# Performance work log

Measured on AMD Instinct MI355X. Metric: run time of the kernel, lower is better.

## Reference

```python
import jax, jax.numpy as jnp
import numpy as np

B, T, D = 16, 2048, 128   # batch, seq_len, input_size
H, L = 256, 2             # hidden_size, rnn layers
N1, N2 = 32, 32           # head output sizes


def _rnn_dir(x, Wih, Whh, bih, bhh, reverse):
    # x: [B, T, din] -> outputs [B, T, H]; torch RNN tanh cell:
    # h_t = tanh(W_ih x_t + b_ih + W_hh h_{t-1} + b_hh), h_0 = 0
    xT = jnp.swapaxes(x, 0, 1)            # [T, B, din]
    if reverse:
        xT = xT[::-1]
    pre = xT @ Wih.T + (bih + bhh)        # batch input projection once
    h0 = jnp.zeros((x.shape[0], Whh.shape[0]), x.dtype)
    def step(h, u):
        h = jnp.tanh(u + h @ Whh.T)
        return h, h
    _, hs = jax.lax.scan(step, h0, pre)   # [T, B, H]
    if reverse:
        hs = hs[::-1]
    return jnp.swapaxes(hs, 0, 1)         # [B, T, H]


def _birnn(x, params):
    out = x
    for l in range(L):
        Wf, Uf, bf, cf, Wb, Ub, bb, cb = params[l]
        fwd = _rnn_dir(out, Wf, Uf, bf, cf, reverse=False)
        bwd = _rnn_dir(out, Wb, Ub, bb, cb, reverse=True)
        out = jnp.concatenate([fwd, bwd], axis=-1)  # [B, T, 2H]
    return out


def _head(h, W1, b1, W2, b2):
    # fc1 -> relu -> fc2, fully batched over [B, T]
    z = jax.nn.relu(jnp.einsum('bth,kh->btk', h, W1) + b1)
    return jnp.einsum('btk,nk->btn', z, W2) + b2


def setup_inputs() -> dict:
    key = jax.random.key(0)
    ks = iter(jax.random.split(key, 40))
    def p(shape):
        return jax.random.normal(next(ks), shape, jnp.float32) * 0.05
    inp = {"x": jax.random.normal(next(ks), (B, T, D), jnp.float32)}
    for l in range(L):
        din = D if l == 0 else 2 * H
        for d in ("f", "b"):
            inp[f"Wih{l}{d}"] = p((H, din))
            inp[f"Whh{l}{d}"] = p((H, H))
            inp[f"bih{l}{d}"] = p((H,))
            inp[f"bhh{l}{d}"] = p((H,))
    for t, n in (("t1", N1), ("t2", N2)):
        inp[f"W1{t}"] = p((H // 2, 2 * H))
        inp[f"b1{t}"] = p((H // 2,))
        inp[f"W2{t}"] = p((n, H // 2))
        inp[f"b2{t}"] = p((n,))
    return inp


def reference(x,
              Wih0f, Whh0f, bih0f, bhh0f, Wih0b, Whh0b, bih0b, bhh0b,
              Wih1f, Whh1f, bih1f, bhh1f, Wih1b, Whh1b, bih1b, bhh1b,
              W1t1, b1t1, W2t1, b2t1, W1t2, b1t2, W2t2, b2t2):
    params = [
        (Wih0f, Whh0f, bih0f, bhh0f, Wih0b, Whh0b, bih0b, bhh0b),
        (Wih1f, Whh1f, bih1f, bhh1f, Wih1b, Whh1b, bih1b, bhh1b),
    ]
    out = _birnn(x, params)                       # [B, T, 2H]
    y1 = _head(out, W1t1, b1t1, W2t1, b2t1)       # [B, T, N1]
    y2 = _head(out, W1t2, b1t2, W2t2, b2t2)       # [B, T, N2]
    return (y1, y2)
```

## Files before the change

kernel.cpp:

```cpp
#include <hip/hip_runtime.h>
#include <hip/hip_fp16.h>

typedef _Float16 half2_t __attribute__((ext_vector_type(2)));
typedef _Float16 half8_t __attribute__((ext_vector_type(8)));
typedef float f32x4 __attribute__((ext_vector_type(4)));

struct __align__(16) H2x4 { half2_t h[4]; };

__device__ __forceinline__ float fdot2f(half2_t a, half2_t b, float c){
#if __has_builtin(__builtin_amdgcn_fdot2)
  return __builtin_amdgcn_fdot2(a, b, c, false);
#else
  return c + (float)a[0]*(float)b[0] + (float)a[1]*(float)b[1];
#endif
}

__device__ __forceinline__ float fast_exp2f(float x){
#if __has_builtin(__builtin_amdgcn_exp2f)
  return __builtin_amdgcn_exp2f(x);
#else
  return __expf(x*0.6931471805599453f);
#endif
}

struct PrepArgs {
  const float* src[13];
  __half* dst[13];
  int n[13];
};
__global__ __launch_bounds__(256) void prep_cast_k(PrepArgs a){
  const int r = blockIdx.y;
  const int n = a.n[r];
  const float* __restrict__ s = a.src[r];
  __half* __restrict__ d = a.dst[r];
  for (int i = blockIdx.x*256 + threadIdx.x; i < n; i += gridDim.x*256)
    d[i] = __float2half(s[i]);
}

struct BiasArgs {
  const float *bih0f,*bhh0f,*bih0b,*bhh0b,*bih1f,*bhh1f,*bih1b,*bhh1b;
  const float *b1t1,*b1t2,*b2t1,*b2t2;
  float *b0,*b1,*bz,*by;
};
__global__ __launch_bounds__(256) void prep_bias_k(BiasArgs a){
  const int i = threadIdx.x;
  if (i < 256){
    a.b0[i]     = a.bih0f[i] + a.bhh0f[i];
    a.b0[256+i] = a.bih0b[i] + a.bhh0b[i];
    a.b1[i]     = a.bih1f[i] + a.bhh1f[i];
    a.b1[256+i] = a.bih1b[i] + a.bhh1b[i];
  }
  if (i < 128){ a.bz[i] = a.b1t1[i]; a.bz[128+i] = a.b1t2[i]; }
  if (i < 32){  a.by[i] = a.b2t1[i]; a.by[32+i]  = a.b2t2[i]; }
}

template<bool RELU>
__global__ __launch_bounds__(256,2) void gemm_nt_k(
    const __half* __restrict__ A, const __half* __restrict__ B,
    __half* __restrict__ C, const float* __restrict__ bias,
    int M, int N, int K, long dirStride)
{
  __shared__ __align__(16) _Float16 As[128*40];
  __shared__ __align__(16) _Float16 Bs[128*40];
  const int tid = threadIdx.x;
  const int wave = tid>>6, lane = tid&63;
  const int wr = wave>>1, wc = wave&1;
  const int lrow = lane&15, lk = lane>>4;
  const int m0 = blockIdx.x*128, n0 = blockIdx.y*128;
  f32x4 acc[4][4];
  #pragma unroll
  for (int i=0;i<4;i++)
    #pragma unroll
    for (int j=0;j<4;j++) acc[i][j] = (f32x4){0.f,0.f,0.f,0.f};

  for (int k0=0; k0<K; k0+=32){
    __syncthreads();
    #pragma unroll
    for (int i=0;i<2;i++){
      int idx = i*256 + tid;
      int row = idx>>2, ch = idx&3;
      const int4 av = *(const int4*)(A + (size_t)(m0+row)*K + k0 + ch*8);
      const int4 bv = *(const int4*)(B + (size_t)(n0+row)*K + k0 + ch*8);
      *(int4*)(As + row*40 + ch*8) = av;
      *(int4*)(Bs + row*40 + ch*8) = bv;
    }
    __syncthreads();
    half8_t af[4], bf[4];
    #pragma unroll
    for (int mi=0;mi<4;mi++) af[mi] = *(const half8_t*)(As + (wr*64+mi*16+lrow)*40 + lk*8);
    #pragma unroll
    for (int ni=0;ni<4;ni++) bf[ni] = *(const half8_t*)(Bs + (wc*64+ni*16+lrow)*40 + lk*8);
    #pragma unroll
    for (int mi=0;mi<4;mi++)
      #pragma unroll
      for (int ni=0;ni<4;ni++)
        acc[mi][ni] = __builtin_amdgcn_mfma_f32_16x16x32_f16(af[mi], bf[ni], acc[mi][ni], 0,0,0);
  }
  #pragma unroll
  for (int mi=0;mi<4;mi++){
    #pragma unroll
    for (int ni=0;ni<4;ni++){
      const int n = n0 + wc*64 + ni*16 + lrow;
      const float bv = bias[n];
      const size_t base = (size_t)(n>>8)*dirStride + (size_t)(n&255);
      #pragma unroll
      for (int r2=0;r2<4;r2++){
        const int m = m0 + wr*64 + mi*16 + lk*4 + r2;
        float v = acc[mi][ni][r2] + bv;
        if (RELU) v = fmaxf(v, 0.f);
        C[(size_t)m*256 + base] = __float2half(v);
      }
    }
  }
}

__global__ __launch_bounds__(256,1) void rnn_layer_k(
    const __half* __restrict__ pre, const __half* __restrict__ whh,
    __half* __restrict__ out, int T)
{
  const int dir = blockIdx.x >> 4;
  const int batch = blockIdx.x & 15;
  const int tid = threadIdx.x;
  half2_t w[128];
  {
    const int4* wp = (const int4*)(whh + dir*65536 + tid*256);
    #pragma unroll
    for (int c=0;c<32;c++){
      H2x4 q = __builtin_bit_cast(H2x4, wp[c]);
      w[4*c+0]=q.h[0]; w[4*c+1]=q.h[1]; w[4*c+2]=q.h[2]; w[4*c+3]=q.h[3];
    }
  }
  __shared__ __align__(16) half2_t hbuf[2][128];
  if (tid < 128){ half2_t z; z[0]=(_Float16)0.f; z[1]=(_Float16)0.f; hbuf[0][tid]=z; }
  const int ttstep = dir ? -256 : 256;
  const int ostep  = dir ? -512 : 512;
  const int t0 = dir ? (T-1) : 0;
  const __half* pcur = pre + (size_t)dir*8388608 + ((size_t)batch*T + t0)*256 + tid;
  __half* ocur = out + ((size_t)batch*T + t0)*512 + dir*256 + tid;
  float u_cur = __half2float(*pcur);
  __syncthreads();
  for (int t=0; t<T; ++t){
    if (t+1 < T) pcur += ttstep;
    const float u_next = __half2float(*pcur);
    float a0=u_cur, a1=0.f, a2=0.f, a3=0.f;
    const H2x4* hb = (const H2x4*)hbuf[t&1];
    #pragma unroll
    for (int c=0;c<32;c++){
      H2x4 hv = hb[c];
      a0 = fdot2f(w[4*c+0], hv.h[0], a0);
      a1 = fdot2f(w[4*c+1], hv.h[1], a1);
      a2 = fdot2f(w[4*c+2], hv.h[2], a2);
      a3 = fdot2f(w[4*c+3], hv.h[3], a3);
    }
    const float x = (a0+a1)+(a2+a3);
    const float e2 = fast_exp2f(x * 2.8853900817779268f);
    const float h  = fmaf(-2.f, __builtin_amdgcn_rcpf(1.f + e2), 1.f);
    *ocur = __float2half(h);
    ocur += ostep;
    const float ho = __shfl_xor(h, 1, 64);
    if (!(tid & 1)){
      half2_t hw; hw[0]=(_Float16)h; hw[1]=(_Float16)ho;
      hbuf[(t&1)^1][tid>>1] = hw;
    }
    u_cur = u_next;
    __syncthreads();
  }
}

__global__ __launch_bounds__(256,4) void head2_k(
    const __half* __restrict__ z, const __half* __restrict__ w2,
    const float* __restrict__ by, float* __restrict__ yout)
{
  __shared__ _Float16 w2s[64*130];
  __shared__ __align__(16) _Float16 zs[4*256];
  const int tid = threadIdx.x;
  {
    const half2_t* g = (const half2_t*)w2;
    for (int idx=tid; idx<4096; idx+=256){
      int row=idx>>6, c=idx&63;
      *(half2_t*)(w2s + row*130 + c*2) = g[idx];
    }
  }
  const int m0 = blockIdx.x*4;
  if (tid < 128){
    const int4* g = (const int4*)(z + (size_t)m0*256);
    *(int4*)(zs + (tid>>5)*256 + (tid&31)*8) = g[tid];
  }
  __syncthreads();
  const int r = tid>>6, n = tid&63;
  const int head = n>>5;
  const half2_t* zp = (const half2_t*)(zs + r*256) + head*64;
  const half2_t* wp = (const half2_t*)(w2s + n*130);
  float acc0=by[n], acc1=0.f;
  #pragma unroll
  for (int j=0;j<64;j+=2){
    acc0 = fdot2f(zp[j],   wp[j],   acc0);
    acc1 = fdot2f(zp[j+1], wp[j+1], acc1);
  }
  yout[(size_t)head*1048576 + (size_t)(m0+r)*32 + (n&31)] = acc0+acc1;
}

extern "C" void kernel_launch(void* const* d_in, const int* in_sizes, int n_in,
                              void* d_out, int out_size, void* d_ws, size_t ws_size,
                              hipStream_t stream)
{
  (void)in_sizes; (void)n_in; (void)out_size; (void)ws_size;
  const float* X    =(const float*)d_in[0];
  const float* Wih0f=(const float*)d_in[1];
  const float* Whh0f=(const float*)d_in[2];
  const float* bih0f=(const float*)d_in[3];
  const float* bhh0f=(const float*)d_in[4];
  const float* Wih0b=(const float*)d_in[5];
  const float* Whh0b=(const float*)d_in[6];
  const float* bih0b=(const float*)d_in[7];
  const float* bhh0b=(const float*)d_in[8];
  const float* Wih1f=(const float*)d_in[9];
  const float* Whh1f=(const float*)d_in[10];
  const float* bih1f=(const float*)d_in[11];
  const float* bhh1f=(const float*)d_in[12];
  const float* Wih1b=(const float*)d_in[13];
  const float* Whh1b=(const float*)d_in[14];
  const float* bih1b=(const float*)d_in[15];
  const float* bhh1b=(const float*)d_in[16];
  const float* W1t1 =(const float*)d_in[17];
  const float* b1t1 =(const float*)d_in[18];
  const float* W2t1 =(const float*)d_in[19];
  const float* b2t1 =(const float*)d_in[20];
  const float* W1t2 =(const float*)d_in[21];
  const float* b1t2 =(const float*)d_in[22];
  const float* W2t2 =(const float*)d_in[23];
  const float* b2t2 =(const float*)d_in[24];

  char* ws = (char*)d_ws;
  size_t off = 0;
  auto alloc = [&](size_t bytes)->void*{ void* p = ws + off; off += (bytes + 1023) & ~(size_t)1023; return p; };
  __half* x16  = (__half*)alloc((size_t)4194304*2);
  __half* wih0 = (__half*)alloc((size_t)65536*2);
  __half* whh0 = (__half*)alloc((size_t)131072*2);
  __half* wih1 = (__half*)alloc((size_t)262144*2);
  __half* whh1 = (__half*)alloc((size_t)131072*2);
  __half* w1   = (__half*)alloc((size_t)131072*2);
  __half* w2   = (__half*)alloc((size_t)8192*2);
  float* b0 = (float*)alloc(512*4);
  float* b1 = (float*)alloc(512*4);
  float* bz = (float*)alloc(256*4);
  float* by = (float*)alloc(64*4);
  __half* preP = (__half*)alloc((size_t)16777216*2);
  __half* out0 = (__half*)alloc((size_t)16777216*2);
  __half* out1 = (__half*)alloc((size_t)16777216*2);

  PrepArgs pa;
  auto set=[&](int r, const float* s, __half* d, int n){ pa.src[r]=s; pa.dst[r]=d; pa.n[r]=n; };
  set(0, X, x16, 4194304);
  set(1, Wih0f, wih0, 32768);       set(2, Wih0b, wih0+32768, 32768);
  set(3, Whh0f, whh0, 65536);       set(4, Whh0b, whh0+65536, 65536);
  set(5, Wih1f, wih1, 131072);      set(6, Wih1b, wih1+131072, 131072);
  set(7, Whh1f, whh1, 65536);       set(8, Whh1b, whh1+65536, 65536);
  set(9, W1t1, w1, 65536);          set(10, W1t2, w1+65536, 65536);
  set(11, W2t1, w2, 4096);          set(12, W2t2, w2+4096, 4096);
  prep_cast_k<<<dim3(1024,13),256,0,stream>>>(pa);

  BiasArgs ba = {bih0f,bhh0f,bih0b,bhh0b,bih1f,bhh1f,bih1b,bhh1b,b1t1,b1t2,b2t1,b2t2,b0,b1,bz,by};
  prep_bias_k<<<1,256,0,stream>>>(ba);

  gemm_nt_k<false><<<dim3(256,4),256,0,stream>>>(x16, wih0, preP, b0, 32768,512,128, 8388608L);
  rnn_layer_k<<<32,256,0,stream>>>(preP, whh0, out0, 2048);
  gemm_nt_k<false><<<dim3(256,4),256,0,stream>>>(out0, wih1, preP, b1, 32768,512,512, 8388608L);
  rnn_layer_k<<<32,256,0,stream>>>(preP, whh1, out1, 2048);
  gemm_nt_k<true><<<dim3(256,2),256,0,stream>>>(out1, w1, preP, bz, 32768,256,512, 0L);
  head2_k<<<8192,256,0,stream>>>(preP, w2, by, (float*)d_out);
}
```

Measured before the change: 2.968 ms.

## Batch RNN recurrence across sequences with MFMA in one block per direction

The recurrent step is rewritten so that one workgroup per direction computes all 16 batch sequences at once with MFMA instructions. The Whh matrix stays in registers as MFMA A-fragments, and the hidden states are shared through an LDS double buffer. The input-projection GEMM epilogue now writes pre-activations in a time-major, MFMA-fragment-friendly layout so each step can load them directly. This replaces 32 blocks of scalar fdot2 work, each with its own per-step barrier, with 2 blocks using matrix cores. The cost is that only two CUs are active during the recurrence, and the output writes are scattered.

```diff
diff --git a/kernel.cpp b/kernel.cpp
--- a/kernel.cpp
+++ b/kernel.cpp
@@ -6,6 +6,7 @@
 typedef float f32x4 __attribute__((ext_vector_type(4)));
 
 struct __align__(16) H2x4 { half2_t h[4]; };
+struct __align__(8)  H2x2 { half2_t h[2]; };
 
 __device__ __forceinline__ float fdot2f(half2_t a, half2_t b, float c){
 #if __has_builtin(__builtin_amdgcn_fdot2)
@@ -54,11 +55,11 @@
   if (i < 32){  a.by[i] = a.b2t1[i]; a.by[32+i]  = a.b2t2[i]; }
 }
 
-template<bool RELU>
+template<int MODE>
 __global__ __launch_bounds__(256,2) void gemm_nt_k(
     const __half* __restrict__ A, const __half* __restrict__ B,
     __half* __restrict__ C, const float* __restrict__ bias,
-    int M, int N, int K, long dirStride)
+    int M, int N, int K)
 {
   __shared__ __align__(16) _Float16 As[128*40];
   __shared__ __align__(16) _Float16 Bs[128*40];
@@ -102,68 +103,107 @@
     for (int ni=0;ni<4;ni++){
       const int n = n0 + wc*64 + ni*16 + lrow;
       const float bv = bias[n];
-      const size_t base = (size_t)(n>>8)*dirStride + (size_t)(n&255);
       #pragma unroll
       for (int r2=0;r2<4;r2++){
         const int m = m0 + wr*64 + mi*16 + lk*4 + r2;
         float v = acc[mi][ni][r2] + bv;
-        if (RELU) v = fmaxf(v, 0.f);
-        C[(size_t)m*256 + base] = __float2half(v);
+        if (MODE==1){
+          C[(size_t)m*256 + n] = __float2half(fmaxf(v, 0.f));
+        } else {
+          const int dir = n>>8, row = n&255;
+          const int b = m>>11, t = m&2047;
+          const size_t di = (((size_t)(dir*2048 + t)*64 + (row>>2))*16 + (size_t)b)*4 + (row&3);
+          C[di] = __float2half(v);
+        }
       }
     }
   }
 }
 
-__global__ __launch_bounds__(256,1) void rnn_layer_k(
-    const __half* __restrict__ pre, const __half* __restrict__ whh,
+__global__ __launch_bounds__(256,1) void rnn_mfma_k(
+    const __half* __restrict__ preM, const __half* __restrict__ whh,
     __half* __restrict__ out, int T)
 {
-  const int dir = blockIdx.x >> 4;
-  const int batch = blockIdx.x & 15;
-  const int tid = threadIdx.x;
-  half2_t w[128];
+  const int dir  = blockIdx.x;
+  const int tid  = threadIdx.x;
+  const int wave = tid>>6, lane = tid&63;
+  const int lb = lane&15;
+  const int lk = lane>>4;
+
+  half8_t af[4][8];
   {
-    const int4* wp = (const int4*)(whh + dir*65536 + tid*256);
-    #pragma unroll
-    for (int c=0;c<32;c++){
-      H2x4 q = __builtin_bit_cast(H2x4, wp[c]);
-      w[4*c+0]=q.h[0]; w[4*c+1]=q.h[1]; w[4*c+2]=q.h[2]; w[4*c+3]=q.h[3];
-    }
-  }
-  __shared__ __align__(16) half2_t hbuf[2][128];
-  if (tid < 128){ half2_t z; z[0]=(_Float16)0.f; z[1]=(_Float16)0.f; hbuf[0][tid]=z; }
-  const int ttstep = dir ? -256 : 256;
-  const int ostep  = dir ? -512 : 512;
-  const int t0 = dir ? (T-1) : 0;
-  const __half* pcur = pre + (size_t)dir*8388608 + ((size_t)batch*T + t0)*256 + tid;
-  __half* ocur = out + ((size_t)batch*T + t0)*512 + dir*256 + tid;
-  float u_cur = __half2float(*pcur);
+    const __half* wp = whh + (size_t)dir*65536;
+    #pragma unroll
+    for (int mt=0;mt<4;++mt)
+      #pragma unroll
+      for (int kt=0;kt<8;++kt)
+        af[mt][kt] = *(const half8_t*)(wp + (size_t)(wave*64 + mt*16 + lb)*256 + kt*32 + lk*8);
+  }
+
+  __shared__ __align__(16) _Float16 hbuf[2][4096];
+  {
+    uint4 z = {0u,0u,0u,0u};
+    *(uint4*)(&hbuf[0][tid*16])     = z;
+    *(uint4*)(&hbuf[0][tid*16 + 8]) = z;
+  }
+  _Float16* cur = &hbuf[0][0];
+  _Float16* nxt = &hbuf[1][0];
+
+  int tt = dir ? (T-1) : 0;
+  const long pstep = dir ? -1024L : 1024L;
+  const uint2* pp = (const uint2*)preM + ((size_t)(dir*T + tt)*64 + wave*16 + lk)*16 + lb;
+  uint2 pcur[4], pnext[4];
+  #pragma unroll
+  for (int mt=0;mt<4;++mt) pcur[mt] = pp[mt*64];
   __syncthreads();
+
   for (int t=0; t<T; ++t){
-    if (t+1 < T) pcur += ttstep;
-    const float u_next = __half2float(*pcur);
-    float a0=u_cur, a1=0.f, a2=0.f, a3=0.f;
-    const H2x4* hb = (const H2x4*)hbuf[t&1];
-    #pragma unroll
-    for (int c=0;c<32;c++){
-      H2x4 hv = hb[c];
-      a0 = fdot2f(w[4*c+0], hv.h[0], a0);
-      a1 = fdot2f(w[4*c+1], hv.h[1], a1);
-      a2 = fdot2f(w[4*c+2], hv.h[2], a2);
-      a3 = fdot2f(w[4*c+3], hv.h[3], a3);
-    }
-    const float x = (a0+a1)+(a2+a3);
-    const float e2 = fast_exp2f(x * 2.8853900817779268f);
-    const float h  = fmaf(-2.f, __builtin_amdgcn_rcpf(1.f + e2), 1.f);
-    *ocur = __float2half(h);
-    ocur += ostep;
-    const float ho = __shfl_xor(h, 1, 64);
-    if (!(tid & 1)){
-      half2_t hw; hw[0]=(_Float16)h; hw[1]=(_Float16)ho;
-      hbuf[(t&1)^1][tid>>1] = hw;
-    }
-    u_cur = u_next;
+    if (t+1 < T){
+      pp += pstep;
+      #pragma unroll
+      for (int mt=0;mt<4;++mt) pnext[mt] = pp[mt*64];
+    }
+    half8_t bf[8];
+    #pragma unroll
+    for (int kt=0;kt<8;++kt)
+      bf[kt] = *(const half8_t*)(cur + (kt*4 + lk)*128 + lb*8);
+    f32x4 a0[4], a1[4];
+    #pragma unroll
+    for (int mt=0;mt<4;++mt){
+      H2x2 q = __builtin_bit_cast(H2x2, pcur[mt]);
+      a0[mt] = (f32x4){(float)q.h[0][0], (float)q.h[0][1], (float)q.h[1][0], (float)q.h[1][1]};
+      a1[mt] = (f32x4){0.f,0.f,0.f,0.f};
+    }
+    #pragma unroll
+    for (int kt=0;kt<4;++kt){
+      #pragma unroll
+      for (int mt=0;mt<4;++mt){
+        a0[mt] = __builtin_amdgcn_mfma_f32_16x16x32_f16(af[mt][kt],   bf[kt],   a0[mt], 0,0,0);
+        a1[mt] = __builtin_amdgcn_mfma_f32_16x16x32_f16(af[mt][kt+4], bf[kt+4], a1[mt], 0,0,0);
+      }
+    }
+    #pragma unroll
+    for (int mt=0;mt<4;++mt){
+      float h[4];
+      #pragma unroll
+      for (int i=0;i<4;++i){
+        const float u  = a0[mt][i] + a1[mt][i];
+        const float e2 = fast_exp2f(u * 2.8853900817779268f);
+        h[i] = fmaf(-2.f, __builtin_amdgcn_rcpf(1.f + e2), 1.f);
+      }
+      half2_t hlo; hlo[0]=(_Float16)h[0]; hlo[1]=(_Float16)h[1];
+      half2_t hhi; hhi[0]=(_Float16)h[2]; hhi[1]=(_Float16)h[3];
+      H2x2 pk2; pk2.h[0]=hlo; pk2.h[1]=hhi;
+      const uint2 pv = __builtin_bit_cast(uint2, pk2);
+      const int row = wave*64 + mt*16 + lk*4;
+      *(uint2*)(out + ((size_t)lb*T + tt)*512 + dir*256 + row) = pv;
+      *(uint2*)(nxt + (wave*8 + mt*2 + (lk>>1))*128 + lb*8 + (lk&1)*4) = pv;
+    }
     __syncthreads();
+    { _Float16* tmp = cur; cur = nxt; nxt = tmp; }
+    #pragma unroll
+    for (int mt=0;mt<4;++mt) pcur[mt] = pnext[mt];
+    tt += dir ? -1 : 1;
   }
 }
 
@@ -245,7 +285,7 @@
   float* b1 = (float*)alloc(512*4);
   float* bz = (float*)alloc(256*4);
   float* by = (float*)alloc(64*4);
-  __half* preP = (__half*)alloc((size_t)16777216*2);
+  __half* preM = (__half*)alloc((size_t)16777216*2);
   __half* out0 = (__half*)alloc((size_t)16777216*2);
   __half* out1 = (__half*)alloc((size_t)16777216*2);
 
@@ -263,10 +303,10 @@
   BiasArgs ba = {bih0f,bhh0f,bih0b,bhh0b,bih1f,bhh1f,bih1b,bhh1b,b1t1,b1t2,b2t1,b2t2,b0,b1,bz,by};
   prep_bias_k<<<1,256,0,stream>>>(ba);
 
-  gemm_nt_k<false><<<dim3(256,4),256,0,stream>>>(x16, wih0, preP, b0, 32768,512,128, 8388608L);
-  rnn_layer_k<<<32,256,0,stream>>>(preP, whh0, out0, 2048);
-  gemm_nt_k<false><<<dim3(256,4),256,0,stream>>>(out0, wih1, preP, b1, 32768,512,512, 8388608L);
-  rnn_layer_k<<<32,256,0,stream>>>(preP, whh1, out1, 2048);
-  gemm_nt_k<true><<<dim3(256,2),256,0,stream>>>(out1, w1, preP, bz, 32768,256,512, 0L);
-  head2_k<<<8192,256,0,stream>>>(preP, w2, by, (float*)d_out);
-}
+  gemm_nt_k<0><<<dim3(256,4),256,0,stream>>>(x16, wih0, preM, b0, 32768,512,128);
+  rnn_mfma_k<<<2,256,0,stream>>>(preM, whh0, out0, 2048);
+  gemm_nt_k<0><<<dim3(256,4),256,0,stream>>>(out0, wih1, preM, b1, 32768,512,512);
+  rnn_mfma_k<<<2,256,0,stream>>>(preM, whh1, out1, 2048);
+  gemm_nt_k<1><<<dim3(256,2),256,0,stream>>>(out1, w1, preM, bz, 32768,256,512);
+  head2_k<<<8192,256,0,stream>>>(preM, w2, by, (float*)d_out);
+}
```

Result: slower. 4.512 ms (+52.0%).
